# Kernel optimization log

Measured on AMD Instinct MI355X. Metric: run time of the kernel, lower is better.

Reference implementation:

```python
import jax, jax.numpy as jnp
import numpy as np

B, T, D = 2, 2048, 2048
N, K, H = 16, 8, 128  # num_heads, num_kv_heads, head_dim
SOFTCAP = 50.0
ROPE_BASE = 10000.0


def apply_rope(x, positions):
    # x: [B, L, heads, H], positions: [B, L]
    head_dim = x.shape[-1]
    fraction = 2.0 * jnp.arange(head_dim // 2, dtype=jnp.float32) / head_dim
    timescale = ROPE_BASE ** fraction  # [H/2]
    sinusoid = positions.astype(jnp.float32)[..., None] / timescale  # [B, L, H/2]
    sinusoid = sinusoid[..., None, :]  # [B, L, 1, H/2]
    sin, cos = jnp.sin(sinusoid), jnp.cos(sinusoid)
    first, second = jnp.split(x, 2, axis=-1)
    out = jnp.concatenate([first * cos - second * sin,
                           second * cos + first * sin], axis=-1)
    return out.astype(x.dtype)


def setup_inputs() -> dict:
    key = jax.random.key(0)
    kx, kq, kkv, ko = jax.random.split(key, 4)
    x = jax.random.normal(kx, (B, T, D), dtype=jnp.float32)
    positions = jnp.broadcast_to(jnp.arange(T, dtype=jnp.int32), (B, T))
    attn_mask = jnp.broadcast_to(
        jnp.tril(jnp.ones((T, T), dtype=bool))[None, None], (B, 1, T, T))
    # variance-scaling fan_in init approximated with scaled normals
    w_q = jax.random.normal(kq, (N, D, H), dtype=jnp.float32) / np.sqrt(D)
    w_kv = jax.random.normal(kkv, (2, K, D, H), dtype=jnp.float32) / np.sqrt(D)
    w_out = jax.random.normal(ko, (N, H, D), dtype=jnp.float32) / np.sqrt(N * H)
    return {"x": x, "positions": positions, "attn_mask": attn_mask,
            "w_q": w_q, "w_kv": w_kv, "w_out": w_out}


def reference(x, positions, attn_mask, w_q, w_kv, w_out):
    # QKV projections (GQA: separate q and kv einsums)
    q = jnp.einsum('BTD,NDH->BTNH', x, w_q)        # [B,T,N,H]
    kv = jnp.einsum('BSD,cKDH->cBSKH', x, w_kv)     # [2,B,S,K,H]
    k, v = kv[0], kv[1]
    q = apply_rope(q, positions) * (H ** -0.5)      # rsqrt_head_dim norm
    k = apply_rope(k, positions)
    # GQA grouping: N = K * G
    G = N // K
    qg = q.reshape(B, T, K, G, H)
    logits = jnp.einsum('BTKGH,BSKH->BKGTS', qg, k).astype(jnp.float32)
    logits = jnp.tanh(logits / SOFTCAP) * SOFTCAP   # logits softcap
    big_neg = -2.3819763e+38
    masked = jnp.where(attn_mask[:, :, None, :, :], logits, big_neg)
    probs = jax.nn.softmax(masked, axis=-1).astype(k.dtype)
    encoded = jnp.einsum('BKGTS,BSKH->BTKGH', probs, v).reshape(B, T, N, H)
    return jnp.einsum('BTNH,NHD->BTD', encoded, w_out)
```

## Files before the change

### kernel.cpp

```cpp
#include <hip/hip_runtime.h>
#include <math.h>
#include <stdint.h>


typedef unsigned short u16;
using bf16x8 = __attribute__((ext_vector_type(8))) short;
using f32x4  = __attribute__((ext_vector_type(4))) float;

#define MFMA_BF16(a,b,c) __builtin_amdgcn_mfma_f32_16x16x32_bf16((a),(b),(c),0,0,0)

static __device__ __forceinline__ float b2f(u16 u) {
  union { unsigned int i; float f; } v; v.i = ((unsigned int)u) << 16; return v.f;
}
static __device__ __forceinline__ u16 f2b(float f) {
  union { float f; unsigned int i; } v; v.f = f;
  unsigned int r = v.i + 0x7fffu + ((v.i >> 16) & 1u);
  return (u16)(r >> 16);
}
static __device__ __forceinline__ unsigned pk2(float x0, float x1) {
  union { float f; unsigned u; } a, b;
  a.f = x0; b.f = x1;
  return __builtin_amdgcn_perm(b.u + 0x8000u, a.u + 0x8000u, 0x07060302u);
}
static __device__ __forceinline__ float rexp2(float a) {
  float r;
  asm("v_exp_f32 %0, %1" : "=v"(r) : "v"(a));
  return r;
}
static __device__ __forceinline__ void gload_lds16(const void* g, void* l) {
  __builtin_amdgcn_global_load_lds((__attribute__((address_space(1))) void*)(g),
                                   (__attribute__((address_space(3))) void*)(l),
                                   16, 0, 0);
}

__global__ __launch_bounds__(256) void prep(const float* __restrict__ x, u16* __restrict__ xb,
                                            const float* __restrict__ wq,
                                            const float* __restrict__ wkv,
                                            const float* __restrict__ wout,
                                            u16* __restrict__ wqkvt, u16* __restrict__ woutt) {
  const int tid = threadIdx.x;
  int bid = blockIdx.x;
  if (bid < 8192) {
    const int i = (bid * 256 + tid) * 4;
    const float4 v = *(const float4*)(x + i);
    ushort4 o;
    o.x = f2b(v.x); o.y = f2b(v.y); o.z = f2b(v.z); o.w = f2b(v.w);
    *(ushort4*)(xb + i) = o;
    return;
  }
  bid -= 8192;
  const float* src;
  u16* dst;
  int rows, cols, bx, by;
  if (bid < 8192) {
    const int seg = bid >> 12;
    const int r = bid & 4095;
    const int mat = r >> 8;
    bx = (r & 255) & 3;
    by = (r & 255) >> 2;
    rows = 2048; cols = 128;
    src = (seg ? wkv : wq) + (size_t)mat * 2048 * 128;
    dst = wqkvt + (size_t)(seg * 16 + mat) * 2048 * 128;
  } else {
    const int r = bid - 8192;
    bx = r & 63;
    by = r >> 6;
    rows = 2048; cols = 2048;
    src = wout;
    dst = woutt;
  }
  __shared__ u16 tile[32][33];
  const int c0 = bx * 32, r0 = by * 32;
  const int tx = tid & 31, ty = tid >> 5;
#pragma unroll
  for (int j = 0; j < 4; ++j)
    tile[ty + j * 8][tx] = f2b(src[(size_t)(r0 + ty + j * 8) * cols + (c0 + tx)]);
  __syncthreads();
#pragma unroll
  for (int j = 0; j < 4; ++j)
    dst[(size_t)(c0 + ty + j * 8) * rows + (r0 + tx)] = tile[tx][ty + j * 8];
}

__global__ __launch_bounds__(512, 2) void gemm_qkv(const u16* __restrict__ X,
                                                   const u16* __restrict__ wqkvt,
                                                   u16* __restrict__ qb,
                                                   u16* __restrict__ kb,
                                                   u16* __restrict__ vtb) {
  __shared__ __align__(16) u16 sAB[2][2][16384];
  const int m0 = blockIdx.x * 256;
  const int ct0 = blockIdx.y * 2;
  const u16* BT = wqkvt + (size_t)blockIdx.y * 256 * 2048;
  const int tid = threadIdx.x;
  const int wave = tid >> 6, lane = tid & 63;
  const int wm = wave >> 2, wn = wave & 3;
  const int quad = lane >> 4, l16 = lane & 15;
  const int srow = lane >> 3;
  const int sch = (lane & 7) ^ srow;

  f32x4 acc[8][4] = {};

  auto STAGE = [&](int kt, int bsel) {
    const int k0 = kt * 64;
#pragma unroll
    for (int s = 0; s < 4; ++s) {
      const int ia = wave * 4 + s;
      const int row = ia * 8 + srow;
      gload_lds16(X + (size_t)(m0 + row) * 2048 + k0 + sch * 8,
                  (char*)&sAB[bsel][0][0] + ia * 1024);
      gload_lds16(BT + (size_t)row * 2048 + k0 + sch * 8,
                  (char*)&sAB[bsel][1][0] + ia * 1024);
    }
  };

  auto COMPUTE = [&](int bsel) {
    const char* aB = (const char*)&sAB[bsel][0][0];
    const char* bB = (const char*)&sAB[bsel][1][0];
#pragma unroll
    for (int ks = 0; ks < 2; ++ks) {
      bf16x8 bfr[4];
#pragma unroll
      for (int nf = 0; nf < 4; ++nf) {
        const int Rb = wn * 64 + nf * 16 + l16;
        bfr[nf] = *(const bf16x8*)(bB + Rb * 128 + (((ks * 4 + quad) ^ (Rb & 7)) << 4));
      }
      __builtin_amdgcn_s_setprio(1);
#pragma unroll
      for (int mf = 0; mf < 8; ++mf) {
        const int R = wm * 128 + mf * 16 + l16;
        const bf16x8 af = *(const bf16x8*)(aB + R * 128 + (((ks * 4 + quad) ^ (R & 7)) << 4));
#pragma unroll
        for (int nf = 0; nf < 4; ++nf)
          acc[mf][nf] = MFMA_BF16(af, bfr[nf], acc[mf][nf]);
      }
      __builtin_amdgcn_s_setprio(0);
    }
  };

  STAGE(0, 0);
#pragma unroll 1
  for (int t = 0; t < 31; ++t) {
    STAGE(t + 1, (t + 1) & 1);
    asm volatile("s_waitcnt vmcnt(8)" ::: "memory");
    __builtin_amdgcn_s_barrier();
    asm volatile("" ::: "memory");
    COMPUTE(t & 1);
    asm volatile("" ::: "memory");
    __builtin_amdgcn_s_barrier();
    asm volatile("" ::: "memory");
  }
  asm volatile("s_waitcnt vmcnt(0)" ::: "memory");
  __builtin_amdgcn_s_barrier();
  asm volatile("" ::: "memory");
  COMPUTE(1);

#pragma unroll
  for (int mf = 0; mf < 8; ++mf) {
    const int mm = m0 + wm * 128 + mf * 16 + quad * 4;
    const int b = mm >> 11;
    const int t = mm & 2047;
#pragma unroll
    for (int nf = 0; nf < 4; ++nf) {
      const int colg = wn * 64 + nf * 16;
      const int ct = ct0 + (colg >> 7);
      const int h = (colg & 127) + l16;
      if (ct < 16) {
        u16* d = qb + (((size_t)b * 16 + ct) * 2048 + t) * 128 + h;
#pragma unroll
        for (int i = 0; i < 4; ++i) d[(size_t)i * 128] = f2b(acc[mf][nf][i]);
      } else if (ct < 24) {
        u16* d = kb + (((size_t)b * 8 + (ct - 16)) * 2048 + t) * 128 + h;
#pragma unroll
        for (int i = 0; i < 4; ++i) d[(size_t)i * 128] = f2b(acc[mf][nf][i]);
      } else {
        u16* d = vtb + (((size_t)b * 8 + (ct - 24)) * 128 + h) * 2048 + t;
        uint2 pkv;
        pkv.x = (unsigned)f2b(acc[mf][nf][0]) | ((unsigned)f2b(acc[mf][nf][1]) << 16);
        pkv.y = (unsigned)f2b(acc[mf][nf][2]) | ((unsigned)f2b(acc[mf][nf][3]) << 16);
        *(uint2*)d = pkv;
      }
    }
  }
}

__global__ __launch_bounds__(256) void rope_kernel(u16* __restrict__ qb,
                                                   u16* __restrict__ kb,
                                                   const int* __restrict__ pos) {
  const unsigned idx = blockIdx.x * 256 + threadIdx.x;
  const unsigned QP = 1u << 21;
  u16* p;
  float scale;
  int b, t, j2;
  if (idx < QP) {
    j2 = (int)(idx & 31) * 2; t = (int)((idx >> 5) & 2047);
    const int hd = (int)((idx >> 16) & 15); b = (int)(idx >> 20);
    p = qb + (((size_t)b * 16 + hd) * 2048 + t) * 128;
    scale = 0.08838834764831845f;
  } else {
    const unsigned r = idx - QP;
    j2 = (int)(r & 31) * 2; t = (int)((r >> 5) & 2047);
    const int hd = (int)((r >> 16) & 7); b = (int)(r >> 19);
    p = kb + (((size_t)b * 8 + hd) * 2048 + t) * 128;
    scale = 1.0f;
  }
  const float fpos = (float)pos[(size_t)b * 2048 + t];
  const unsigned lo = *(const unsigned*)(p + j2);
  const unsigned hi = *(const unsigned*)(p + j2 + 64);
  unsigned olo = 0, ohi = 0;
#pragma unroll
  for (int d = 0; d < 2; ++d) {
    const int j = j2 + d;
    const float ts = __powf(10000.0f, (float)j * (1.0f / 64.0f));
    float sn, cs;
    sincosf(fpos / ts, &sn, &cs);
    const float a = b2f((u16)((d ? (lo >> 16) : lo) & 0xffffu));
    const float c2 = b2f((u16)((d ? (hi >> 16) : hi) & 0xffffu));
    olo |= ((unsigned)f2b((a * cs - c2 * sn) * scale)) << (16 * d);
    ohi |= ((unsigned)f2b((c2 * cs + a * sn) * scale)) << (16 * d);
  }
  *(unsigned*)(p + j2) = olo;
  *(unsigned*)(p + j2 + 64) = ohi;
}

__global__ __launch_bounds__(256, 4) void attn_fused(const u16* __restrict__ qg,
                                                     const u16* __restrict__ kg,
                                                     const u16* __restrict__ vtg,
                                                     u16* __restrict__ enc) {
  __shared__ __align__(16) char lds[32768];
  char* sK = lds;
  char* sV = lds + 16384;

  const int bid = blockIdx.x;
  const int half = bid >> 9;
  const int r = bid & 511;
  const int x = r & 7;
  const int g = r >> 3;
  const int pr = g & 15;
  const int head = (g >> 4) * 8 + x;
  const int Q = half ? pr : (31 - pr);
  const int b = head >> 4;
  const int n = head & 15;
  const int kh = n >> 1;

  const u16* qbase = qg + ((size_t)b * 16 + n) * 2048 * 128;
  const u16* kbase = kg + ((size_t)b * 8 + kh) * 2048 * 128;
  const u16* vbase = vtg + ((size_t)b * 8 + kh) * 128 * 2048;

  const int tid = threadIdx.x, wave = tid >> 6, lane = tid & 63;
  const int quad = lane >> 4, l16 = lane & 15;
  const int bp_a0 = ((quad & 1) * 32 + l16) * 4;
  const int bp_a1 = bp_a0 + 64;

  const float L2E = 1.4426950408889634f;
  const float C50 = 72.13475204444817f;
  const float B1 = 1.9235933879e-4f;
  const float B2 = 3.0777494206e-8f;
  const float B3 = 4.9830224200e-12f;

  const u16* kp[4];
  const u16* vp[4];
#pragma unroll
  for (int s = 0; s < 4; ++s) {
    const int kr = wave * 16 + s * 4 + quad;
    kp[s] = kbase + (size_t)kr * 128 + (l16 ^ (s * 4 + quad)) * 8;
    const int vr = wave * 32 + s * 8 + (lane >> 3);
    vp[s] = vbase + (size_t)vr * 2048 + ((lane & 7) ^ (lane >> 3)) * 8;
  }

  const int tw = Q * 64 + wave * 16;
  const int tlane = tw + l16;

  bf16x8 qf[4];
#pragma unroll
  for (int kf = 0; kf < 4; ++kf)
    qf[kf] = *(const bf16x8*)(qbase + (size_t)tlane * 128 + kf * 32 + quad * 8);

  f32x4 o[8] = {};
  f32x4 lacc = {0.f, 0.f, 0.f, 0.f};

#pragma unroll 1
  for (int si = 0; si <= Q; ++si) {
    const int s0 = si * 64;
    __syncthreads();
#pragma unroll
    for (int s = 0; s < 4; ++s) {
      gload_lds16(kp[s], sK + (wave * 4 + s) * 1024);
      gload_lds16(vp[s], sV + (wave * 4 + s) * 1024);
      kp[s] += 64 * 128;
      vp[s] += 64;
    }
    __syncthreads();

    const bool diag = (si == Q);
    const int nfmax = diag ? wave : 3;
    const int kmax = diag ? (wave >> 1) : 1;

    f32x4 sacc[4];
#pragma unroll
    for (int nf = 0; nf < 4; ++nf) {
      if (nf <= nfmax) {
        const int sr = nf * 16 + l16;
        f32x4 a = {0.f, 0.f, 0.f, 0.f};
#pragma unroll
        for (int kf = 0; kf < 4; ++kf) {
          const bf16x8 kfr =
              *(const bf16x8*)(sK + sr * 256 + (((kf * 4 + quad) ^ (sr & 15)) << 4));
          a = MFMA_BF16(kfr, qf[kf], a);
        }
        sacc[nf] = a;
      }
    }

#pragma unroll
    for (int nf = 0; nf < 4; ++nf) {
      if (nf <= nfmax) {
        const f32x4 xv = sacc[nf];
        const f32x4 u = xv * xv;
        f32x4 t = u * (-B3) + B2;
        t = u * t + (-B1);
        t = u * t + L2E;
        f32x4 pv;
#pragma unroll
        for (int i = 0; i < 4; ++i) pv[i] = rexp2(fmaf(xv[i], t[i], -C50));
        if (diag) {
#pragma unroll
          for (int i = 0; i < 4; ++i) {
            const int sg = s0 + nf * 16 + quad * 4 + i;
            if (sg > tlane) pv[i] = 0.0f;
          }
        }
        sacc[nf] = pv;
        lacc += pv;
      }
    }

    unsigned pkd[4][2];
#pragma unroll
    for (int nf = 0; nf < 4; ++nf) {
      if (nf <= nfmax) {
        pkd[nf][0] = pk2(sacc[nf][0], sacc[nf][1]);
        pkd[nf][1] = pk2(sacc[nf][2], sacc[nf][3]);
      } else {
        pkd[nf][0] = 0u; pkd[nf][1] = 0u;
      }
    }

#pragma unroll
    for (int c2 = 0; c2 < 2; ++c2) {
      if (c2 <= kmax) {
        const int lo = (quad >> 1);
        const int dA0 = __builtin_amdgcn_ds_bpermute(bp_a0, (int)pkd[2 * c2][0]);
        const int dB0 = __builtin_amdgcn_ds_bpermute(bp_a0, (int)pkd[2 * c2 + 1][0]);
        const int dA1 = __builtin_amdgcn_ds_bpermute(bp_a0, (int)pkd[2 * c2][1]);
        const int dB1 = __builtin_amdgcn_ds_bpermute(bp_a0, (int)pkd[2 * c2 + 1][1]);
        const int dA2 = __builtin_amdgcn_ds_bpermute(bp_a1, (int)pkd[2 * c2][0]);
        const int dB2 = __builtin_amdgcn_ds_bpermute(bp_a1, (int)pkd[2 * c2 + 1][0]);
        const int dA3 = __builtin_amdgcn_ds_bpermute(bp_a1, (int)pkd[2 * c2][1]);
        const int dB3 = __builtin_amdgcn_ds_bpermute(bp_a1, (int)pkd[2 * c2 + 1][1]);
        union { int d[4]; bf16x8 v; } pb;
        pb.d[0] = lo ? dB0 : dA0;
        pb.d[1] = lo ? dB1 : dA1;
        pb.d[2] = lo ? dB2 : dA2;
        pb.d[3] = lo ? dB3 : dA3;
#pragma unroll
        for (int nfo = 0; nfo < 8; ++nfo) {
          const int hr = nfo * 16 + l16;
          const bf16x8 vb =
              *(const bf16x8*)(sV + hr * 128 + (((c2 * 4 + quad) ^ (hr & 7)) << 4));
          o[nfo] = MFMA_BF16(vb, pb.v, o[nfo]);
        }
      }
    }
  }

  float lsum = lacc[0] + lacc[1] + lacc[2] + lacc[3];
  lsum += __shfl_xor(lsum, 16);
  lsum += __shfl_xor(lsum, 32);
  const float inv = 1.0f / lsum;
  u16* d = enc + (((size_t)b * 2048 + tlane) * 16 + n) * 128 + quad * 4;
#pragma unroll
  for (int nfo = 0; nfo < 8; ++nfo) {
    uint2 st;
    st.x = (unsigned)f2b(o[nfo][0] * inv) | ((unsigned)f2b(o[nfo][1] * inv) << 16);
    st.y = (unsigned)f2b(o[nfo][2] * inv) | ((unsigned)f2b(o[nfo][3] * inv) << 16);
    *(uint2*)(d + nfo * 16) = st;
  }
}

__global__ __launch_bounds__(512, 2) void gemm_out(const u16* __restrict__ A,
                                                   const u16* __restrict__ Bt,
                                                   float* __restrict__ C) {
  __shared__ __align__(16) u16 sA[2][16384];
  __shared__ __align__(16) u16 sB[2][8192];
  const int m0 = blockIdx.x * 256;
  const int n0 = blockIdx.y * 128;
  const int tid = threadIdx.x;
  const int wave = tid >> 6, lane = tid & 63;
  const int wm = wave >> 2, wn = wave & 3;
  const int quad = lane >> 4, l16 = lane & 15;
  const int srow = lane >> 3;
  const int sch = (lane & 7) ^ srow;

  f32x4 acc[8][2] = {};

  auto STAGE = [&](int kt, int bsel) {
    const int k0 = kt * 64;
#pragma unroll
    for (int s = 0; s < 4; ++s) {
      const int ia = wave * 4 + s;
      const int row = ia * 8 + srow;
      gload_lds16(A + (size_t)(m0 + row) * 2048 + k0 + sch * 8,
                  (char*)&sA[bsel][0] + ia * 1024);
    }
#pragma unroll
    for (int s = 0; s < 2; ++s) {
      const int ib = wave * 2 + s;
      const int row = ib * 8 + srow;
      gload_lds16(Bt + (size_t)(n0 + row) * 2048 + k0 + sch * 8,
                  (char*)&sB[bsel][0] + ib * 1024);
    }
  };

  auto COMPUTE = [&](int bsel) {
    const char* aB = (const char*)&sA[bsel][0];
    const char* bB = (const char*)&sB[bsel][0];
#pragma unroll
    for (int ks = 0; ks < 2; ++ks) {
      bf16x8 bfr[2];
#pragma unroll
      for (int nf = 0; nf < 2; ++nf) {
        const int Rb = wn * 32 + nf * 16 + l16;
        bfr[nf] = *(const bf16x8*)(bB + Rb * 128 + (((ks * 4 + quad) ^ (Rb & 7)) << 4));
      }
      __builtin_amdgcn_s_setprio(1);
#pragma unroll
      for (int mf = 0; mf < 8; ++mf) {
        const int R = wm * 128 + mf * 16 + l16;
        const bf16x8 af = *(const bf16x8*)(aB + R * 128 + (((ks * 4 + quad) ^ (R & 7)) << 4));
#pragma unroll
        for (int nf = 0; nf < 2; ++nf)
          acc[mf][nf] = MFMA_BF16(af, bfr[nf], acc[mf][nf]);
      }
      __builtin_amdgcn_s_setprio(0);
    }
  };

  STAGE(0, 0);
#pragma unroll 1
  for (int t = 0; t < 31; ++t) {
    STAGE(t + 1, (t + 1) & 1);
    asm volatile("s_waitcnt vmcnt(6)" ::: "memory");
    __builtin_amdgcn_s_barrier();
    asm volatile("" ::: "memory");
    COMPUTE(t & 1);
    asm volatile("" ::: "memory");
    __builtin_amdgcn_s_barrier();
    asm volatile("" ::: "memory");
  }
  asm volatile("s_waitcnt vmcnt(0)" ::: "memory");
  __builtin_amdgcn_s_barrier();
  asm volatile("" ::: "memory");
  COMPUTE(1);

#pragma unroll
  for (int mf = 0; mf < 8; ++mf) {
    const int mm = m0 + wm * 128 + mf * 16 + quad * 4;
#pragma unroll
    for (int nf = 0; nf < 2; ++nf) {
      const int col = n0 + wn * 32 + nf * 16 + l16;
#pragma unroll
      for (int i = 0; i < 4; ++i) C[(size_t)(mm + i) * 2048 + col] = acc[mf][nf][i];
    }
  }
}

extern "C" void kernel_launch(void* const* d_in, const int* in_sizes, int n_in,
                              void* d_out, int out_size, void* d_ws, size_t ws_size,
                              hipStream_t stream) {
  (void)in_sizes; (void)n_in; (void)out_size; (void)ws_size;
  const float* x     = (const float*)d_in[0];
  const int*   posi  = (const int*)d_in[1];
  const float* w_q   = (const float*)d_in[3];
  const float* w_kv  = (const float*)d_in[4];
  const float* w_out = (const float*)d_in[5];
  float* out = (float*)d_out;

  u16* ws = (u16*)d_ws;
  u16* wqkvt = ws;
  u16* woutt = ws + (size_t)8388608;
  u16* qb    = ws + (size_t)12582912;
  u16* kb    = ws + (size_t)20971520;
  u16* vtb   = ws + (size_t)25165824;
  u16* encb  = ws + (size_t)29360128;
  u16* xb    = encb;

  prep<<<20480, 256, 0, stream>>>(x, xb, w_q, w_kv, w_out, wqkvt, woutt);
  gemm_qkv<<<dim3(16, 16), 512, 0, stream>>>(xb, wqkvt, qb, kb, vtb);
  rope_kernel<<<12288, 256, 0, stream>>>(qb, kb, posi);
  attn_fused<<<1024, 256, 0, stream>>>(qb, kb, vtb, encb);
  gemm_out<<<dim3(16, 16), 512, 0, stream>>>(encb, woutt, out);
}
```

Measured before the change: 358.0 us.

## Register-prefetch next K/V tile to overlap global loads with attention compute

Replaces the direct global-to-LDS loads in the attention loop with a register-staged software pipeline. The next K/V tile is loaded into registers while the current tile is computed, then written to LDS after a barrier, so global memory latency is hidden behind MFMA work. This costs extra VGPRs (eight uint4 per thread), which may hurt occupancy under launch_bounds(256,4). The RoPE kernel also replaces a powf and a division with one exp2f and a multiply when computing the rotation angle.

```diff
diff --git a/kernel.cpp b/kernel.cpp
--- a/kernel.cpp
+++ b/kernel.cpp
@@ -209,9 +209,9 @@
 #pragma unroll
   for (int d = 0; d < 2; ++d) {
     const int j = j2 + d;
-    const float ts = __powf(10000.0f, (float)j * (1.0f / 64.0f));
+    const float ang = fpos * exp2f((float)j * -0.2076205059304601f);
     float sn, cs;
-    sincosf(fpos / ts, &sn, &cs);
+    sincosf(ang, &sn, &cs);
     const float a = b2f((u16)((d ? (lo >> 16) : lo) & 0xffffu));
     const float c2 = b2f((u16)((d ? (hi >> 16) : hi) & 0xffffu));
     olo |= ((unsigned)f2b((a * cs - c2 * sn) * scale)) << (16 * d);
@@ -266,6 +266,25 @@
     vp[s] = vbase + (size_t)vr * 2048 + ((lane & 7) ^ (lane >> 3)) * 8;
   }
 
+  uint4 krg[4], vrg[4];
+  auto LOADREGS = [&]() {
+#pragma unroll
+    for (int s = 0; s < 4; ++s) {
+      krg[s] = *(const uint4*)kp[s];
+      vrg[s] = *(const uint4*)vp[s];
+      kp[s] += 64 * 128;
+      vp[s] += 64;
+    }
+  };
+  auto DSWRITE = [&]() {
+    const int lo16 = lane * 16;
+#pragma unroll
+    for (int s = 0; s < 4; ++s) {
+      *(uint4*)(sK + (wave * 4 + s) * 1024 + lo16) = krg[s];
+      *(uint4*)(sV + (wave * 4 + s) * 1024 + lo16) = vrg[s];
+    }
+  };
+
   const int tw = Q * 64 + wave * 16;
   const int tlane = tw + l16;
 
@@ -276,19 +295,20 @@
 
   f32x4 o[8] = {};
   f32x4 lacc = {0.f, 0.f, 0.f, 0.f};
+
+  LOADREGS();
 
 #pragma unroll 1
   for (int si = 0; si <= Q; ++si) {
     const int s0 = si * 64;
-    __syncthreads();
-#pragma unroll
-    for (int s = 0; s < 4; ++s) {
-      gload_lds16(kp[s], sK + (wave * 4 + s) * 1024);
-      gload_lds16(vp[s], sV + (wave * 4 + s) * 1024);
-      kp[s] += 64 * 128;
-      vp[s] += 64;
-    }
-    __syncthreads();
+    asm volatile("s_waitcnt vmcnt(0)" ::: "memory");
+    __builtin_amdgcn_s_barrier();
+    asm volatile("" ::: "memory");
+    DSWRITE();
+    if (si < Q) LOADREGS();
+    asm volatile("s_waitcnt lgkmcnt(0)" ::: "memory");
+    __builtin_amdgcn_s_barrier();
+    asm volatile("" ::: "memory");
 
     const bool diag = (si == Q);
     const int nfmax = diag ? wave : 3;
```

Result: slower. 483.2 us (+35.0%).
